# Kernel tuning notes

Measured on AMD Instinct MI355X. Metric: run time of the kernel, lower is better.

The kernel has to match this reference:

```python
import jax, jax.numpy as jnp
import numpy as np

ALPHA, BETA, GAMMA, DELTA = 1.0, 1.0, 0.5, 0.3


def setup_inputs() -> dict:
    key = jax.random.key(0)
    k1, k2, k3, k4, k5 = jax.random.split(key, 5)
    B, R = 1024, 192
    return {
        "position_updates": jax.random.uniform(k1, (B, R, 2), dtype=jnp.float32),
        "size_updates": jax.random.uniform(k2, (B, R, 2), dtype=jnp.float32),
        "target_positions": jax.random.uniform(k3, (B, R, 2), dtype=jnp.float32),
        "target_sizes": jax.random.uniform(k4, (B, R, 2), dtype=jnp.float32),
        "adjacency_matrix": jax.random.randint(k5, (1, R, R), 0, 2, dtype=jnp.int32),
    }


def reference(position_updates, size_updates, target_positions, target_sizes, adjacency_matrix):
    # MSE terms
    position_loss = jnp.mean((position_updates - target_positions) ** 2)
    size_loss = jnp.mean((size_updates - target_sizes) ** 2)

    R = position_updates.shape[1]
    triu = jnp.triu(jnp.ones((R, R), dtype=bool), k=1)  # pairs i<j

    # Pairwise overlap penalty, vectorized over all (i, j) pairs.
    x = position_updates[..., 0]  # [B, R]
    y = position_updates[..., 1]
    w = size_updates[..., 0]
    h = size_updates[..., 1]
    # [B, R, R] broadcasted pairwise intersections
    ow = jnp.clip(jnp.minimum((x + w)[:, :, None], (x + w)[:, None, :])
                  - jnp.maximum(x[:, :, None], x[:, None, :]), 0)
    oh = jnp.clip(jnp.minimum((y + h)[:, :, None], (y + h)[:, None, :])
                  - jnp.maximum(y[:, :, None], y[:, None, :]), 0)
    overlap_area = ow * oh  # [B, R, R]
    overlap_penalty = jnp.sum(jnp.where(triu, overlap_area.mean(axis=0), 0.0))

    # Adjacency loss: distance between centers of adjacent rooms (adj from batch 0)
    centers = position_updates + size_updates / 2  # [B, R, 2]
    cx, cy = centers[..., 0], centers[..., 1]
    dx = cx[:, :, None] - cx[:, None, :]
    dy = cy[:, :, None] - cy[:, None, :]
    sq = dx * dx + dy * dy  # [B, R, R]
    adj_mask = triu & (adjacency_matrix[0] > 0)  # [R, R]
    dist = jnp.sqrt(jnp.where(adj_mask[None, :, :], sq, 1.0))  # safe sqrt
    adjacency_loss = jnp.sum(jnp.where(adj_mask, dist.mean(axis=0), 0.0))

    total_loss = (ALPHA * position_loss + BETA * size_loss
                  + GAMMA * overlap_penalty + DELTA * adjacency_loss)
    return (total_loss, position_loss, size_loss, overlap_penalty, adjacency_loss)
```

## Files before the change

### kernel.cpp

```cpp
#include <hip/hip_runtime.h>

#define R 192
#define BATCH 1024
#define TILE 16
#define NT (R / TILE)
#define NBITWORDS (R * 6)


__global__ __launch_bounds__(256) void build_mask_kernel(
    const int* __restrict__ adj, float* __restrict__ ws)
{
    unsigned int* wsbits = (unsigned int*)(ws + 4);
    const int e = blockIdx.x * 256 + threadIdx.x;
    if (e < 4) ws[e] = 0.0f;
    if (e >= R * R) return;
    const int i = e / R;
    const int j = e - i * R;
    const bool pred = (adj[e] > 0) && (j > i);
    const unsigned long long m = __ballot(pred);
    const int lane = e & 63;
    if (lane == 0)  wsbits[e >> 5] = (unsigned int)m;
    if (lane == 32) wsbits[e >> 5] = (unsigned int)(m >> 32);
}

__global__ __launch_bounds__(256) void floorplan_main_kernel(
    const float* __restrict__ pos,
    const float* __restrict__ siz,
    const float* __restrict__ tpos,
    const float* __restrict__ tsiz,
    float* __restrict__ ws)
{
    __shared__ float4 room[R];
    __shared__ unsigned int sadj[NBITWORDS];
    __shared__ float wsum[4][4];

    const int b   = blockIdx.x;
    const int sel = blockIdx.y;
    const int tid = threadIdx.x;

    const float2* pb  = (const float2*)(pos  + (size_t)b * (R * 2));
    const float2* sb  = (const float2*)(siz  + (size_t)b * (R * 2));
    const float2* tpb = (const float2*)(tpos + (size_t)b * (R * 2));
    const float2* tsb = (const float2*)(tsiz + (size_t)b * (R * 2));
    const unsigned int* wsbits = (const unsigned int*)(ws + 4);

    float mse_p = 0.0f, mse_s = 0.0f;

    if (tid < R) {
        float2 p  = pb[tid];
        float2 s  = sb[tid];
        float2 tp = tpb[tid];
        float2 ts = tsb[tid];
        float dpx = p.x - tp.x, dpy = p.y - tp.y;
        float dsx = s.x - ts.x, dsy = s.y - ts.y;
        mse_p = dpx * dpx + dpy * dpy;
        mse_s = dsx * dsx + dsy * dsy;
        room[tid] = make_float4(p.x, p.y, s.x, s.y);
    }
    for (int w = tid; w < NBITWORDS; w += 256) sadj[w] = wsbits[w];
    __syncthreads();

    if (sel != 0) { mse_p = 0.0f; mse_s = 0.0f; }

    float ov = 0.0f, ad = 0.0f;
    const int li = tid >> 4;
    const int lj = tid & 15;

    for (int ti = 0; ti < NT; ++ti) {
        const int   i  = ti * TILE + li;
        const float4 ri = room[i];
        const float xi  = ri.x, yi = ri.y;
        const float xiw = ri.x + ri.z;
        const float yih = ri.y + ri.w;
        const float cxi = fmaf(0.5f, ri.z, ri.x);
        const float cyi = fmaf(0.5f, ri.w, ri.y);
        const unsigned int* rowbits = &sadj[i * 6];

        for (int tj = ti + sel; tj < NT; tj += 2) {
            const int j = tj * TILE + lj;
            const float4 rj = room[j];
            float ow = fminf(xiw, rj.x + rj.z) - fmaxf(xi, rj.x);
            float oh = fminf(yih, rj.y + rj.w) - fmaxf(yi, rj.y);
            ow = fmaxf(ow, 0.0f);
            oh = fmaxf(oh, 0.0f);
            float area = ow * oh;
            ov += (i < j) ? area : 0.0f;

            unsigned int wbits = rowbits[tj >> 1];
            unsigned int bit = (wbits >> (((tj & 1) << 4) + lj)) & 1u;
            float dx = cxi - fmaf(0.5f, rj.z, rj.x);
            float dy = cyi - fmaf(0.5f, rj.w, rj.y);
            float sq = fmaf(dx, dx, dy * dy);
            float d  = __builtin_amdgcn_sqrtf(sq);
            ad += bit ? d : 0.0f;
        }
    }

    for (int off = 32; off > 0; off >>= 1) {
        mse_p += __shfl_down(mse_p, off);
        mse_s += __shfl_down(mse_s, off);
        ov    += __shfl_down(ov, off);
        ad    += __shfl_down(ad, off);
    }
    const int wid  = tid >> 6;
    const int lane = tid & 63;
    if (lane == 0) {
        wsum[wid][0] = mse_p;
        wsum[wid][1] = mse_s;
        wsum[wid][2] = ov;
        wsum[wid][3] = ad;
    }
    __syncthreads();
    if (tid < 4) {
        float v = wsum[0][tid] + wsum[1][tid] + wsum[2][tid] + wsum[3][tid];
        atomicAdd(&ws[tid], v);
    }
}

__global__ void finalize_kernel(const float* __restrict__ ws, float* __restrict__ out) {
    if (threadIdx.x == 0 && blockIdx.x == 0) {
        const float invN = 1.0f / (float)(BATCH * R * 2);
        const float invB = 1.0f / (float)BATCH;
        float pos_loss  = ws[0] * invN;
        float size_loss = ws[1] * invN;
        float overlap   = ws[2] * invB;
        float adjl      = ws[3] * invB;
        out[0] = pos_loss + size_loss + 0.5f * overlap + 0.3f * adjl;
        out[1] = pos_loss;
        out[2] = size_loss;
        out[3] = overlap;
        out[4] = adjl;
    }
}

extern "C" void kernel_launch(void* const* d_in, const int* in_sizes, int n_in,
                              void* d_out, int out_size, void* d_ws, size_t ws_size,
                              hipStream_t stream) {
    const float* pos  = (const float*)d_in[0];
    const float* siz  = (const float*)d_in[1];
    const float* tpos = (const float*)d_in[2];
    const float* tsiz = (const float*)d_in[3];
    const int*   adj  = (const int*)d_in[4];
    float* ws  = (float*)d_ws;
    float* out = (float*)d_out;

    hipLaunchKernelGGL(build_mask_kernel, dim3((R * R + 255) / 256), dim3(256), 0, stream,
                       adj, ws);
    hipLaunchKernelGGL(floorplan_main_kernel, dim3(BATCH, 2), dim3(256), 0, stream,
                       pos, siz, tpos, tsiz, ws);
    hipLaunchKernelGGL(finalize_kernel, dim3(1), dim3(1), 0, stream, ws, out);
}
```

Before: 101.1 us.

## Transpose rooms to batch-major layout and parallelize pairs across batch lanes

Adds a kernel that computes the MSE terms and writes the room data transposed to [room][batch] in workspace. A new pairs kernel maps threads to batch elements and blocks to row i, then loops j>i, so global loads are coalesced and the lower triangle is no longer computed. The adjacency sqrt moves behind a uniform branch on the mask bit, which is warp-uniform because i and j are shared by the whole block. The cost is an extra launch and a round-trip of the transposed data through global memory. Rows with small i also do much more work than rows near the end, so block work is unbalanced.

```diff
diff --git a/kernel.cpp b/kernel.cpp
--- a/kernel.cpp
+++ b/kernel.cpp
@@ -2,118 +2,113 @@
 
 #define R 192
 #define BATCH 1024
-#define TILE 16
-#define NT (R / TILE)
-#define NBITWORDS (R * 6)
+#define RCH 8
 
+#define MASK_OFF_W 4
+#define ROOMT_OFF_B 8192
 
-__global__ __launch_bounds__(256) void build_mask_kernel(
+__global__ __launch_bounds__(256) void prep_kernel(
     const int* __restrict__ adj, float* __restrict__ ws)
 {
-    unsigned int* wsbits = (unsigned int*)(ws + 4);
+    unsigned int* bits = (unsigned int*)(ws + MASK_OFF_W);
     const int e = blockIdx.x * 256 + threadIdx.x;
     if (e < 4) ws[e] = 0.0f;
     if (e >= R * R) return;
     const int i = e / R;
     const int j = e - i * R;
-    const bool pred = (adj[e] > 0) && (j > i);
-    const unsigned long long m = __ballot(pred);
+    const unsigned long long m = __ballot((adj[e] > 0) && (j > i));
     const int lane = e & 63;
-    if (lane == 0)  wsbits[e >> 5] = (unsigned int)m;
-    if (lane == 32) wsbits[e >> 5] = (unsigned int)(m >> 32);
+    if (lane == 0)  bits[e >> 5] = (unsigned int)m;
+    if (lane == 32) bits[e >> 5] = (unsigned int)(m >> 32);
 }
 
-__global__ __launch_bounds__(256) void floorplan_main_kernel(
-    const float* __restrict__ pos,
-    const float* __restrict__ siz,
-    const float* __restrict__ tpos,
-    const float* __restrict__ tsiz,
+__global__ __launch_bounds__(256) void transpose_mse_kernel(
+    const float* __restrict__ pos, const float* __restrict__ siz,
+    const float* __restrict__ tpos, const float* __restrict__ tsiz,
     float* __restrict__ ws)
 {
-    __shared__ float4 room[R];
-    __shared__ unsigned int sadj[NBITWORDS];
-    __shared__ float wsum[4][4];
+    __shared__ float wsum[4][2];
+    float4* roomT = (float4*)((char*)ws + ROOMT_OFF_B);
+    const int tid = threadIdx.x;
+    const int b   = blockIdx.x * 256 + tid;
+    const int r0  = blockIdx.y * RCH;
 
-    const int b   = blockIdx.x;
-    const int sel = blockIdx.y;
-    const int tid = threadIdx.x;
+    const float2* pb  = (const float2*)pos  + (size_t)b * R;
+    const float2* sb  = (const float2*)siz  + (size_t)b * R;
+    const float2* tpb = (const float2*)tpos + (size_t)b * R;
+    const float2* tsb = (const float2*)tsiz + (size_t)b * R;
 
-    const float2* pb  = (const float2*)(pos  + (size_t)b * (R * 2));
-    const float2* sb  = (const float2*)(siz  + (size_t)b * (R * 2));
-    const float2* tpb = (const float2*)(tpos + (size_t)b * (R * 2));
-    const float2* tsb = (const float2*)(tsiz + (size_t)b * (R * 2));
-    const unsigned int* wsbits = (const unsigned int*)(ws + 4);
-
-    float mse_p = 0.0f, mse_s = 0.0f;
-
-    if (tid < R) {
-        float2 p  = pb[tid];
-        float2 s  = sb[tid];
-        float2 tp = tpb[tid];
-        float2 ts = tsb[tid];
+    float mp = 0.0f, ms = 0.0f;
+    #pragma unroll
+    for (int k = 0; k < RCH; ++k) {
+        const int r = r0 + k;
+        float2 p  = pb[r];
+        float2 s  = sb[r];
+        float2 tp = tpb[r];
+        float2 ts = tsb[r];
         float dpx = p.x - tp.x, dpy = p.y - tp.y;
         float dsx = s.x - ts.x, dsy = s.y - ts.y;
-        mse_p = dpx * dpx + dpy * dpy;
-        mse_s = dsx * dsx + dsy * dsy;
-        room[tid] = make_float4(p.x, p.y, s.x, s.y);
+        mp += dpx * dpx + dpy * dpy;
+        ms += dsx * dsx + dsy * dsy;
+        roomT[r * BATCH + b] = make_float4(p.x, p.y, s.x, s.y);
     }
-    for (int w = tid; w < NBITWORDS; w += 256) sadj[w] = wsbits[w];
+
+    for (int off = 32; off > 0; off >>= 1) {
+        mp += __shfl_down(mp, off);
+        ms += __shfl_down(ms, off);
+    }
+    const int wid = tid >> 6, lane = tid & 63;
+    if (lane == 0) { wsum[wid][0] = mp; wsum[wid][1] = ms; }
     __syncthreads();
+    if (tid < 2) {
+        float v = wsum[0][tid] + wsum[1][tid] + wsum[2][tid] + wsum[3][tid];
+        atomicAdd(&ws[tid], v);
+    }
+}
 
-    if (sel != 0) { mse_p = 0.0f; mse_s = 0.0f; }
+__global__ __launch_bounds__(256) void pairs_kernel(float* __restrict__ ws)
+{
+    __shared__ float wsum[4][2];
+    const float4* __restrict__ roomT = (const float4*)((const char*)ws + ROOMT_OFF_B);
+    const unsigned int* __restrict__ bits = (const unsigned int*)(ws + MASK_OFF_W);
+
+    const int tid = threadIdx.x;
+    const int b   = blockIdx.x * 256 + tid;
+    const int i   = blockIdx.y;
+
+    const float4 ri = roomT[i * BATCH + b];
+    const float xi  = ri.x, yi = ri.y;
+    const float xiw = ri.x + ri.z;
+    const float yih = ri.y + ri.w;
+    const float cxi = fmaf(0.5f, ri.z, ri.x);
+    const float cyi = fmaf(0.5f, ri.w, ri.y);
+    const unsigned int* rowbits = bits + i * 6;
 
     float ov = 0.0f, ad = 0.0f;
-    const int li = tid >> 4;
-    const int lj = tid & 15;
-
-    for (int ti = 0; ti < NT; ++ti) {
-        const int   i  = ti * TILE + li;
-        const float4 ri = room[i];
-        const float xi  = ri.x, yi = ri.y;
-        const float xiw = ri.x + ri.z;
-        const float yih = ri.y + ri.w;
-        const float cxi = fmaf(0.5f, ri.z, ri.x);
-        const float cyi = fmaf(0.5f, ri.w, ri.y);
-        const unsigned int* rowbits = &sadj[i * 6];
-
-        for (int tj = ti + sel; tj < NT; tj += 2) {
-            const int j = tj * TILE + lj;
-            const float4 rj = room[j];
-            float ow = fminf(xiw, rj.x + rj.z) - fmaxf(xi, rj.x);
-            float oh = fminf(yih, rj.y + rj.w) - fmaxf(yi, rj.y);
-            ow = fmaxf(ow, 0.0f);
-            oh = fmaxf(oh, 0.0f);
-            float area = ow * oh;
-            ov += (i < j) ? area : 0.0f;
-
-            unsigned int wbits = rowbits[tj >> 1];
-            unsigned int bit = (wbits >> (((tj & 1) << 4) + lj)) & 1u;
+    for (int j = i + 1; j < R; ++j) {
+        const float4 rj = roomT[j * BATCH + b];
+        float ow = fminf(xiw, rj.x + rj.z) - fmaxf(xi, rj.x);
+        float oh = fminf(yih, rj.y + rj.w) - fmaxf(yi, rj.y);
+        ow = fmaxf(ow, 0.0f);
+        oh = fmaxf(oh, 0.0f);
+        ov += ow * oh;
+        if ((rowbits[j >> 5] >> (j & 31)) & 1u) {
             float dx = cxi - fmaf(0.5f, rj.z, rj.x);
             float dy = cyi - fmaf(0.5f, rj.w, rj.y);
-            float sq = fmaf(dx, dx, dy * dy);
-            float d  = __builtin_amdgcn_sqrtf(sq);
-            ad += bit ? d : 0.0f;
+            ad += __builtin_amdgcn_sqrtf(fmaf(dx, dx, dy * dy));
         }
     }
 
     for (int off = 32; off > 0; off >>= 1) {
-        mse_p += __shfl_down(mse_p, off);
-        mse_s += __shfl_down(mse_s, off);
-        ov    += __shfl_down(ov, off);
-        ad    += __shfl_down(ad, off);
+        ov += __shfl_down(ov, off);
+        ad += __shfl_down(ad, off);
     }
-    const int wid  = tid >> 6;
-    const int lane = tid & 63;
-    if (lane == 0) {
-        wsum[wid][0] = mse_p;
-        wsum[wid][1] = mse_s;
-        wsum[wid][2] = ov;
-        wsum[wid][3] = ad;
-    }
+    const int wid = tid >> 6, lane = tid & 63;
+    if (lane == 0) { wsum[wid][0] = ov; wsum[wid][1] = ad; }
     __syncthreads();
-    if (tid < 4) {
+    if (tid < 2) {
         float v = wsum[0][tid] + wsum[1][tid] + wsum[2][tid] + wsum[3][tid];
-        atomicAdd(&ws[tid], v);
+        atomicAdd(&ws[2 + tid], v);
     }
 }
 
@@ -144,9 +139,10 @@
     float* ws  = (float*)d_ws;
     float* out = (float*)d_out;
 
-    hipLaunchKernelGGL(build_mask_kernel, dim3((R * R + 255) / 256), dim3(256), 0, stream,
+    hipLaunchKernelGGL(prep_kernel, dim3((R * R + 255) / 256), dim3(256), 0, stream,
                        adj, ws);
-    hipLaunchKernelGGL(floorplan_main_kernel, dim3(BATCH, 2), dim3(256), 0, stream,
+    hipLaunchKernelGGL(transpose_mse_kernel, dim3(BATCH / 256, R / RCH), dim3(256), 0, stream,
                        pos, siz, tpos, tsiz, ws);
+    hipLaunchKernelGGL(pairs_kernel, dim3(BATCH / 256, R - 1), dim3(256), 0, stream, ws);
     hipLaunchKernelGGL(finalize_kernel, dim3(1), dim3(1), 0, stream, ws, out);
 }
```

Result: slower. 109.0 us (+7.8%).
